# Kernel tuning notes

Measured on AMD Instinct MI355X. Metric: run time of the kernel, lower is better.

## Reference

```python
import jax, jax.numpy as jnp
import numpy as np

NUM_HEADS = 8
NEG_INF = float(-2**32 + 1)  # matches torch padding value -2**32+1


def positional_encoding(B, T, d):
    # matches module: pe[:, :, 0::2] = sin(pos*div), pe[:, :, 1::2] = cos(pos*div)
    pos = jnp.arange(T, dtype=jnp.float32)[:, None]                      # (T, 1)
    div = jnp.exp(jnp.arange(0, d, 2, dtype=jnp.float32) * (-np.log(10000.0) / d))  # (d/2,)
    ang = pos * div                                                       # (T, d/2)
    pe = jnp.zeros((T, d), jnp.float32)
    pe = pe.at[:, 0::2].set(jnp.sin(ang)).at[:, 1::2].set(jnp.cos(ang))
    return jnp.broadcast_to(pe[None], (B, T, d))


def setup_inputs() -> dict:
    key = jax.random.key(0)
    ks = jax.random.split(key, 8)
    B, T, d, dff = 4, 2048, 128, 512
    s = 1.0 / np.sqrt(d)
    return {
        "x": jax.random.normal(ks[0], (B, T, d), jnp.float32),
        "W_Q": jax.random.normal(ks[1], (d, d), jnp.float32) * s,
        "W_K": jax.random.normal(ks[2], (d, d), jnp.float32) * s,
        "W_V": jax.random.normal(ks[3], (d, d), jnp.float32) * s,
        "W1": jax.random.normal(ks[4], (d, dff), jnp.float32) * s,
        "b1": jnp.zeros((dff,), jnp.float32),
        "W2": jax.random.normal(ks[5], (dff, d), jnp.float32) * (1.0 / np.sqrt(dff)),
        "b2": jnp.zeros((d,), jnp.float32),
    }


def reference(x, W_Q, W_K, W_V, W1, b1, W2, b2):
    B, T, d = x.shape
    H = NUM_HEADS
    e = d // H
    x = x + positional_encoding(B, T, d)           # residual later uses post-PE input
    Q = x @ W_Q
    K = x @ W_K
    V = x @ W_V
    # torch split(dim=2)+cat(dim=0) == (b t (h e)) -> (h b) t e; keep head axis separate
    Qh = Q.reshape(B, T, H, e).transpose(2, 0, 1, 3)   # (H, B, T, e)
    Kh = K.reshape(B, T, H, e).transpose(2, 0, 1, 3)
    Vh = V.reshape(B, T, H, e).transpose(2, 0, 1, 3)
    scores = jnp.einsum('hbqe,hbke->hbqk', Qh, Kh) / (T ** 0.5)  # scale by sqrt(time_step)
    mask = jnp.tril(jnp.ones((T, T), jnp.float32))
    scores = jnp.where(mask == 0, jnp.float32(NEG_INF), scores)
    # torch F.softmax(dim=1) on (H*B, T, T) -> softmax over QUERY axis (axis=2 here)
    attn = jax.nn.softmax(scores, axis=2)
    out = jnp.einsum('hbqk,hbke->hbqe', attn, Vh)      # (H, B, T, e)
    out = out.transpose(1, 2, 0, 3).reshape(B, T, d)   # cat heads back on feature dim
    ff = jnp.maximum(out @ W1 + b1, 0.0) @ W2 + b2
    return ff + x
```

## Files before the change

### kernel.cpp

```cpp
#include <hip/hip_runtime.h>
#include <math.h>
#include <stdint.h>

#define T_SEQ 2048
#define BATCH 4
#define DMODEL 128
#define DFF 512
#define NHEAD 8
#define EHEAD 16

#define QSCALE (0.022097086912079608f * 1.4426950408889634f)

typedef __attribute__((ext_vector_type(8))) short bf16x8;
typedef __attribute__((ext_vector_type(4))) short bf16x4;
typedef __attribute__((ext_vector_type(4))) float f32x4;

__device__ __forceinline__ short f2bf(float f) {
    uint32_t u = __float_as_uint(f);
    u = u + 0x7FFF + ((u >> 16) & 1);
    return (short)(u >> 16);
}
__device__ __forceinline__ short bftrunc(float f) {
    return (short)(__float_as_uint(f) >> 16);
}
__device__ __forceinline__ float bf2f(short s) {
    return __uint_as_float(((uint32_t)(unsigned short)s) << 16);
}
__device__ __forceinline__ float exp2_fast(float x) {
#if __has_builtin(__builtin_amdgcn_exp2f)
    return __builtin_amdgcn_exp2f(x);
#else
    float r; asm("v_exp_f32 %0, %1" : "=v"(r) : "v"(x)); return r;
#endif
}

#define MFMA16(A, B, C) __builtin_amdgcn_mfma_f32_16x16x32_bf16(A, B, C, 0, 0, 0)

__device__ __forceinline__ void gload16(const void* g, void* l) {
    __builtin_amdgcn_global_load_lds(
        (const __attribute__((address_space(1))) void*)g,
        (__attribute__((address_space(3))) void*)l, 16, 0, 0);
}

__device__ __forceinline__ int quad_rank(int id) {
    int group = id >> 8, pos = id & 255;
    return (group & 1) ? (((group + 1) << 8) - 1 - pos) : ((group << 8) + pos);
}

#define WP 136
__global__ __launch_bounds__(256) void k_qkv(const float* __restrict__ x,
                                             const float* __restrict__ WQ,
                                             const float* __restrict__ WK,
                                             const float* __restrict__ WV,
                                             const float* __restrict__ W1,
                                             const float* __restrict__ W2,
                                             float* __restrict__ xpe,
                                             short* __restrict__ Qh,
                                             short* __restrict__ Kh,
                                             short* __restrict__ Vs,
                                             short* __restrict__ W1t,
                                             short* __restrict__ W2t) {
    __shared__ __align__(16) short Wlds[128 * WP];
    int z = blockIdx.y;
    int tid = threadIdx.x;

    if (z == 3) {
        int base = (int)blockIdx.x * 256 + tid;
#pragma unroll
        for (int i = 0; i < 2; ++i) {
            int o = base + i * 32768;
            int n = o >> 7, k = o & 127;
            W1t[o] = f2bf(W1[k * 512 + n]);
        }
#pragma unroll
        for (int i = 0; i < 2; ++i) {
            int o = base + i * 32768;
            int n = o >> 9, k = o & 511;
            W2t[o] = f2bf(W2[k * 128 + n]);
        }
        return;
    }

    int wave = tid >> 6, lane = tid & 63;
    int g = lane >> 4, c = lane & 15;
    int row0 = blockIdx.x * 64 + wave * 16;
    int row = row0 + c;
    int tloc = row & (T_SEQ - 1);

    {
        const float* Wsrc = (z == 0) ? WQ : (z == 1) ? WK : WV;
        int k = tid & 127, n0 = (tid >> 7) * 64;
        const float* src = Wsrc + k * 128 + n0;
#pragma unroll
        for (int j = 0; j < 64; j += 4) {
            float4 wv = *(const float4*)(src + j);
            Wlds[(n0 + j + 0) * WP + k] = f2bf(wv.x);
            Wlds[(n0 + j + 1) * WP + k] = f2bf(wv.y);
            Wlds[(n0 + j + 2) * WP + k] = f2bf(wv.z);
            Wlds[(n0 + j + 3) * WP + k] = f2bf(wv.w);
        }
    }

    bf16x8 af[4];
#pragma unroll
    for (int kk = 0; kk < 4; ++kk) {
        int d0 = kk * 32 + 8 * g;
        const float* xb = x + (size_t)row * 128 + d0;
        float4 xa = *(const float4*)(xb);
        float4 xc = *(const float4*)(xb + 4);
        float vv[8] = {xa.x, xa.y, xa.z, xa.w, xc.x, xc.y, xc.z, xc.w};
#pragma unroll
        for (int p = 0; p < 4; ++p) {
            int d = d0 + 2 * p;
            float dv = __expf(-(float)d * (9.210340371976184f / 128.0f));
            float ang = (float)tloc * dv;
            vv[2 * p] += __sinf(ang);
            vv[2 * p + 1] += __cosf(ang);
        }
        if (z == 0) {
            float* xo = xpe + (size_t)row * 128 + d0;
            *(float4*)(xo) = make_float4(vv[0], vv[1], vv[2], vv[3]);
            *(float4*)(xo + 4) = make_float4(vv[4], vv[5], vv[6], vv[7]);
        }
#pragma unroll
        for (int j = 0; j < 8; ++j) af[kk][j] = f2bf(vv[j]);
    }
    __syncthreads();

    bf16x8 wf[8][4];
#pragma unroll
    for (int nt = 0; nt < 8; ++nt)
#pragma unroll
        for (int kk = 0; kk < 4; ++kk)
            wf[nt][kk] = *(const bf16x8*)(&Wlds[(nt * 16 + c) * WP + kk * 32 + 8 * g]);

    f32x4 acc[8];
#pragma unroll
    for (int nt = 0; nt < 8; ++nt) acc[nt] = (f32x4){0.f, 0.f, 0.f, 0.f};
#pragma unroll
    for (int kk = 0; kk < 4; ++kk)
#pragma unroll
        for (int nt = 0; nt < 8; ++nt)
            acc[nt] = MFMA16(af[kk], wf[nt][kk], acc[nt]);

    int b = row0 >> 11;
    int t0 = (row0 & (T_SEQ - 1)) + 4 * g;
    if (z < 2) {
        short* dst = (z == 0) ? Qh : Kh;
        float sc = (z == 0) ? QSCALE : 1.0f;
#pragma unroll
        for (int nt = 0; nt < 8; ++nt) {
            int hb = nt * 4 + b;
#pragma unroll
            for (int r = 0; r < 4; ++r)
                dst[(size_t)(hb * T_SEQ + t0 + r) * 16 + c] = f2bf(acc[nt][r] * sc);
        }
    } else {
#pragma unroll
        for (int nt = 0; nt < 8; ++nt) {
            int hb = nt * 4 + b;
            bf16x4 v;
#pragma unroll
            for (int r = 0; r < 4; ++r) v[r] = f2bf(acc[nt][r]);
            *(bf16x4*)(Vs + (size_t)(hb * 16 + c) * T_SEQ + t0) = v;
        }
    }
}
#undef WP

__global__ __launch_bounds__(256, 4) void k_csum(const short* __restrict__ Qh,
                                                 const short* __restrict__ Kh,
                                                 short* __restrict__ Vs) {
    __shared__ __align__(16) short Qt[2][4096];
    __shared__ float csLds[4][32];
    __shared__ float invl[64];
    const bf16x8 zz = {0, 0, 0, 0, 0, 0, 0, 0};
    const f32x4 z = {0.f, 0.f, 0.f, 0.f};

    int rank = quad_rank((int)blockIdx.x);
    int kc = rank >> 5, hb = rank & 31;
    int tid = threadIdx.x;
    int wave = tid >> 6, lane = tid & 63;
    int g = lane >> 4, c = lane & 15;
    int s = wave & 1, h = wave >> 1;
    int kw = kc * 64 + s * 32;
    const size_t hbT = (size_t)hb * T_SEQ;
    const short* Qg = Qh + hbT * 16;

    bf16x8 kfA = zz, kfB = zz;
    if (g < 2) {
        kfA = *(const bf16x8*)(Kh + (hbT + kw + c) * 16 + 8 * g);
        kfB = *(const bf16x8*)(Kh + (hbT + kw + 16 + c) * 16 + 8 * g);
    }

#define QSTAGE(bf, tq)                                                       \
    do {                                                                     \
        const short* src = Qg + (size_t)(tq) * 4096;                         \
        gload16(src + tid * 8, &Qt[bf][tid * 8]);                            \
        gload16(src + 2048 + tid * 8, &Qt[bf][2048 + tid * 8]);              \
    } while (0)

    int tstart = kc >> 2;
    QSTAGE(0, tstart);
    __syncthreads();

    float csA = 0.f, csB = 0.f;
    for (int t = tstart; t < 8; ++t) {
        int buf = (t - tstart) & 1;
        if (t + 1 < 8) QSTAGE(buf ^ 1, t + 1);
        const short* Qtb = &Qt[buf][0];
#pragma unroll
        for (int sj = 0; sj < 4; ++sj) {
            int ss = 4 * h + sj;
            int q32 = t * 256 + ss * 32;
            if (q32 + 31 < kw) continue;
            bf16x8 qfa = zz, qfb = zz;
            if (g < 2) {
                qfa = *(const bf16x8*)(Qtb + (ss * 32 + c) * 16 + g * 8);
                qfb = *(const bf16x8*)(Qtb + (ss * 32 + 16 + c) * 16 + g * 8);
            }
            f32x4 sA1 = MFMA16(qfa, kfA, z);
            f32x4 sB1 = MFMA16(qfa, kfB, z);
            f32x4 sA2 = MFMA16(qfb, kfA, z);
            f32x4 sB2 = MFMA16(qfb, kfB, z);
            if (q32 >= kw + 32) {
#pragma unroll
                for (int r = 0; r < 4; ++r) {
                    csA += exp2_fast(sA1[r]) + exp2_fast(sA2[r]);
                    csB += exp2_fast(sB1[r]) + exp2_fast(sB2[r]);
                }
            } else {
                int kA = kw + c, kB = kw + 16 + c;
#pragma unroll
                for (int r = 0; r < 4; ++r) {
                    int qa = q32 + 4 * g + r, qb = q32 + 16 + 4 * g + r;
                    csA += (qa >= kA) ? exp2_fast(sA1[r]) : 0.f;
                    csA += (qb >= kA) ? exp2_fast(sA2[r]) : 0.f;
                    csB += (qa >= kB) ? exp2_fast(sB1[r]) : 0.f;
                    csB += (qb >= kB) ? exp2_fast(sB2[r]) : 0.f;
                }
            }
        }
        __syncthreads();
    }
#undef QSTAGE

    csA += __shfl_xor(csA, 16);
    csA += __shfl_xor(csA, 32);
    csB += __shfl_xor(csB, 16);
    csB += __shfl_xor(csB, 32);
    if (lane < 32) csLds[wave][lane] = (lane < 16) ? csA : csB;
    __syncthreads();
    if (tid < 64) {
        int st = tid >> 5, col = tid & 31;
        invl[tid] = 1.0f / (csLds[st][col] + csLds[st + 2][col]);
    }
    __syncthreads();
    if (tid < 128) {
        int e = tid >> 3, kcol = (tid & 7) * 8;
        size_t vo = (size_t)(hb * 16 + e) * T_SEQ + kc * 64 + kcol;
        bf16x8 v = *(bf16x8*)(Vs + vo);
        bf16x8 o;
#pragma unroll
        for (int j = 0; j < 8; ++j) o[j] = f2bf(bf2f(v[j]) * invl[kcol + j]);
        *(bf16x8*)(Vs + vo) = o;
    }
}

__global__ __launch_bounds__(256, 4) void k_attn(const short* __restrict__ Qh,
                                                 const short* __restrict__ Kh,
                                                 const short* __restrict__ Vs,
                                                 short* __restrict__ AObf) {
    __shared__ __align__(16) short Kt[2][4096];
    __shared__ __align__(16) short Vt[2][4096];
    const bf16x8 zz = {0, 0, 0, 0, 0, 0, 0, 0};
    const f32x4 z = {0.f, 0.f, 0.f, 0.f};

    int rank = quad_rank((int)blockIdx.x);
    int qn = 31 - (rank >> 5), hb = rank & 31;
    int h2 = hb >> 2, b = hb & 3;
    int tid = threadIdx.x;
    int wave = tid >> 6, lane = tid & 63;
    int g = lane >> 4, c = lane & 15;
    int s = wave & 1, h = wave >> 1;
    int q0w = qn * 64 + s * 32;
    const size_t hbT = (size_t)hb * T_SEQ;
    const short* Kg = Kh + hbT * 16;
    const short* Vg = Vs + (size_t)hb * 16 * T_SEQ;

    bf16x8 qf0 = zz, qf1 = zz;
    if (g < 2) {
        qf0 = *(const bf16x8*)(Qh + (hbT + q0w + c) * 16 + 8 * g);
        qf1 = *(const bf16x8*)(Qh + (hbT + q0w + 16 + c) * 16 + 8 * g);
    }

    int nT = (qn >> 2) + 1;

#define STAGE(bf, kt)                                                        \
    do {                                                                     \
        int k0s = (kt) * 256;                                                \
        gload16(Kg + (size_t)k0s * 16 + tid * 8, &Kt[bf][tid * 8]);          \
        gload16(Kg + (size_t)k0s * 16 + 2048 + tid * 8,                      \
                &Kt[bf][2048 + tid * 8]);                                    \
        int e0 = tid >> 5, j0 = (tid & 31) ^ (e0 & 7);                       \
        gload16(Vg + (size_t)e0 * T_SEQ + k0s + j0 * 8, &Vt[bf][tid * 8]);   \
        int s1_ = tid + 256;                                                 \
        int e1 = s1_ >> 5, j1 = (s1_ & 31) ^ (e1 & 7);                       \
        gload16(Vg + (size_t)e1 * T_SEQ + k0s + j1 * 8,                      \
                &Vt[bf][2048 + tid * 8]);                                    \
    } while (0)

    STAGE(0, 0);
    __syncthreads();

    f32x4 acc0 = z, acc1 = z;
    for (int t = 0; t < nT; ++t) {
        int buf = t & 1;
        if (t + 1 < nT) STAGE(buf ^ 1, t + 1);
        const short* Ktb = &Kt[buf][0];
        const short* Vtb = &Vt[buf][0];
#pragma unroll
        for (int sj = 0; sj < 4; ++sj) {
            int ss = 4 * h + sj;
            int k32 = t * 256 + ss * 32;
            if (k32 > q0w + 31) continue;
            bf16x8 kf0 = zz, kf1 = zz;
            if (g < 2) {
                kf0 = *(const bf16x8*)(Ktb + (ss * 32 + c) * 16 + g * 8);
                kf1 = *(const bf16x8*)(Ktb + (ss * 32 + 16 + c) * 16 + g * 8);
            }
            int ja = ss * 4 + (g >> 1);
            const short* vrow = Vtb + c * 256 + ((g & 1) << 2);
            bf16x4 v0 = *(const bf16x4*)(vrow + ((ja ^ (c & 7)) << 3));
            bf16x4 v1 = *(const bf16x4*)(vrow + (((ja + 2) ^ (c & 7)) << 3));
            f32x4 s0 = MFMA16(kf0, qf0, z);
            f32x4 s1 = MFMA16(kf1, qf0, z);
            f32x4 s2 = MFMA16(kf0, qf1, z);
            f32x4 s3 = MFMA16(kf1, qf1, z);
            bf16x8 aA, aB, vf;
            if (k32 + 31 <= q0w) {
#pragma unroll
                for (int r = 0; r < 4; ++r) {
                    aA[r] = bftrunc(exp2_fast(s0[r]));
                    aA[4 + r] = bftrunc(exp2_fast(s1[r]));
                    aB[r] = bftrunc(exp2_fast(s2[r]));
                    aB[4 + r] = bftrunc(exp2_fast(s3[r]));
                    vf[r] = v0[r];
                    vf[4 + r] = v1[r];
                }
            } else {
                int qa = q0w + c, qb = q0w + 16 + c;
                int ka = k32 + 4 * g, kb = k32 + 16 + 4 * g;
#pragma unroll
                for (int r = 0; r < 4; ++r) {
                    aA[r] = (ka + r <= qa) ? bftrunc(exp2_fast(s0[r])) : (short)0;
                    aA[4 + r] = (kb + r <= qa) ? bftrunc(exp2_fast(s1[r])) : (short)0;
                    aB[r] = (ka + r <= qb) ? bftrunc(exp2_fast(s2[r])) : (short)0;
                    aB[4 + r] = (kb + r <= qb) ? bftrunc(exp2_fast(s3[r])) : (short)0;
                    vf[r] = v0[r];
                    vf[4 + r] = v1[r];
                }
            }
            acc0 = MFMA16(aA, vf, acc0);
            acc1 = MFMA16(aB, vf, acc1);
        }
        __syncthreads();
    }
#undef STAGE

    float* Of = (float*)&Kt[0][0];
    if (h == 1) {
#pragma unroll
        for (int r = 0; r < 4; ++r) {
            Of[r * 128 + s * 64 + lane] = acc0[r];
            Of[(4 + r) * 128 + s * 64 + lane] = acc1[r];
        }
    }
    __syncthreads();
    if (h == 0) {
#pragma unroll
        for (int r = 0; r < 4; ++r) {
            acc0[r] += Of[r * 128 + s * 64 + lane];
            acc1[r] += Of[(4 + r) * 128 + s * 64 + lane];
        }
#pragma unroll
        for (int r = 0; r < 4; ++r) {
            AObf[(size_t)(b * T_SEQ + q0w + 4 * g + r) * DMODEL + h2 * EHEAD + c] = f2bf(acc0[r]);
            AObf[(size_t)(b * T_SEQ + q0w + 16 + 4 * g + r) * DMODEL + h2 * EHEAD + c] = f2bf(acc1[r]);
        }
    }
}

__global__ __launch_bounds__(256) void k_ff(const short* __restrict__ AObf,
                                            const short* __restrict__ W1t,
                                            const float* __restrict__ b1,
                                            const short* __restrict__ W2t,
                                            const float* __restrict__ b2,
                                            const float* __restrict__ xpe,
                                            float* __restrict__ out) {
    __shared__ __align__(16) short Fl[32][516];
    int w = threadIdx.x >> 6, lane = threadIdx.x & 63;
    int g = lane >> 4, c = lane & 15;
    int row0 = blockIdx.x * 32;

    {
        bf16x8 wf[8][4];
#pragma unroll
        for (int nt = 0; nt < 8; ++nt)
#pragma unroll
            for (int kk = 0; kk < 4; ++kk)
                wf[nt][kk] = *(const bf16x8*)(W1t + (w * 128 + nt * 16 + c) * 128 + kk * 32 + 8 * g);

#pragma unroll
        for (int ch = 0; ch < 2; ++ch) {
            int rbase = row0 + ch * 16;
            bf16x8 af[4];
#pragma unroll
            for (int kk = 0; kk < 4; ++kk)
                af[kk] = *(const bf16x8*)(AObf + (size_t)(rbase + c) * 128 + kk * 32 + 8 * g);

            f32x4 acc[8];
#pragma unroll
            for (int nt = 0; nt < 8; ++nt) acc[nt] = (f32x4){0.f, 0.f, 0.f, 0.f};
#pragma unroll
            for (int kk = 0; kk < 4; ++kk)
#pragma unroll
                for (int nt = 0; nt < 8; ++nt)
                    acc[nt] = MFMA16(af[kk], wf[nt][kk], acc[nt]);

#pragma unroll
            for (int nt = 0; nt < 8; ++nt) {
                int col = w * 128 + nt * 16 + c;
                float bb = b1[col];
#pragma unroll
                for (int r = 0; r < 4; ++r)
                    Fl[ch * 16 + 4 * g + r][col] = f2bf(fmaxf(acc[nt][r] + bb, 0.f));
            }
        }
    }
    __syncthreads();

    bf16x8 wf2[2][16];
#pragma unroll
    for (int nt = 0; nt < 2; ++nt)
#pragma unroll
        for (int kk = 0; kk < 16; ++kk)
            wf2[nt][kk] = *(const bf16x8*)(W2t + (w * 32 + nt * 16 + c) * 512 + kk * 32 + 8 * g);

#pragma unroll
    for (int ch = 0; ch < 2; ++ch) {
        int rbase = row0 + ch * 16;
        f32x4 acc2[2];
        acc2[0] = (f32x4){0.f, 0.f, 0.f, 0.f};
        acc2[1] = (f32x4){0.f, 0.f, 0.f, 0.f};
#pragma unroll
        for (int kk = 0; kk < 16; ++kk) {
            bf16x8 a = *(const bf16x8*)(&Fl[ch * 16 + c][kk * 32 + 8 * g]);
            acc2[0] = MFMA16(a, wf2[0][kk], acc2[0]);
            acc2[1] = MFMA16(a, wf2[1][kk], acc2[1]);
        }
#pragma unroll
        for (int nt = 0; nt < 2; ++nt) {
            int col = w * 32 + nt * 16 + c;
            float bb = b2[col];
#pragma unroll
            for (int r = 0; r < 4; ++r) {
                size_t o = (size_t)(rbase + 4 * g + r) * DMODEL + col;
                out[o] = acc2[nt][r] + bb + xpe[o];
            }
        }
    }
}

extern "C" void kernel_launch(void* const* d_in, const int* in_sizes, int n_in,
                              void* d_out, int out_size, void* d_ws, size_t ws_size,
                              hipStream_t stream) {
    const float* x  = (const float*)d_in[0];
    const float* WQ = (const float*)d_in[1];
    const float* WK = (const float*)d_in[2];
    const float* WV = (const float*)d_in[3];
    const float* W1 = (const float*)d_in[4];
    const float* b1 = (const float*)d_in[5];
    const float* W2 = (const float*)d_in[6];
    const float* b2 = (const float*)d_in[7];
    float* out = (float*)d_out;

    const size_t NTD = (size_t)BATCH * T_SEQ * DMODEL;
    float* xpe   = (float*)d_ws;
    short* Qh    = (short*)(xpe + NTD);
    short* Kh    = Qh + NTD;
    short* Vs    = Kh + NTD;
    short* AObf  = Vs + NTD;
    short* W1t   = AObf + NTD;
    short* W2t   = W1t + 65536;

    k_qkv<<<dim3(128, 4), dim3(256), 0, stream>>>(x, WQ, WK, WV, W1, W2,
                                                  xpe, Qh, Kh, Vs, W1t, W2t);

    k_csum<<<dim3(1024), dim3(256), 0, stream>>>(Qh, Kh, Vs);

    k_attn<<<dim3(1024), dim3(256), 0, stream>>>(Qh, Kh, Vs, AObf);

    k_ff<<<dim3(256), dim3(256), 0, stream>>>(AObf, W1t, b1, W2t, b2, xpe, out);
}
```

Before: 55.08 us.

## Halve per-block work in csum and attention kernels, doubling grid to 2048 blocks

```diff
diff --git a/kernel.cpp b/kernel.cpp
--- a/kernel.cpp
+++ b/kernel.cpp
@@ -42,7 +42,7 @@
         (__attribute__((address_space(3))) void*)l, 16, 0, 0);
 }
 
-__device__ __forceinline__ int quad_rank(int id) {
+__device__ __forceinline__ int oct_rank(int id) {
     int group = id >> 8, pos = id & 255;
     return (group & 1) ? (((group + 1) << 8) - 1 - pos) : ((group << 8) + pos);
 }
@@ -173,17 +173,16 @@
                                                  short* __restrict__ Vs) {
     __shared__ __align__(16) short Qt[2][4096];
     __shared__ float csLds[4][32];
-    __shared__ float invl[64];
+    __shared__ float invl[32];
     const bf16x8 zz = {0, 0, 0, 0, 0, 0, 0, 0};
     const f32x4 z = {0.f, 0.f, 0.f, 0.f};
 
-    int rank = quad_rank((int)blockIdx.x);
+    int rank = oct_rank((int)blockIdx.x);
     int kc = rank >> 5, hb = rank & 31;
     int tid = threadIdx.x;
     int wave = tid >> 6, lane = tid & 63;
     int g = lane >> 4, c = lane & 15;
-    int s = wave & 1, h = wave >> 1;
-    int kw = kc * 64 + s * 32;
+    int kw = kc * 32;
     const size_t hbT = (size_t)hb * T_SEQ;
     const short* Qg = Qh + hbT * 16;
 
@@ -200,7 +199,7 @@
         gload16(src + 2048 + tid * 8, &Qt[bf][2048 + tid * 8]);              \
     } while (0)
 
-    int tstart = kc >> 2;
+    int tstart = kc >> 3;
     QSTAGE(0, tstart);
     __syncthreads();
 
@@ -210,8 +209,8 @@
         if (t + 1 < 8) QSTAGE(buf ^ 1, t + 1);
         const short* Qtb = &Qt[buf][0];
 #pragma unroll
-        for (int sj = 0; sj < 4; ++sj) {
-            int ss = 4 * h + sj;
+        for (int sj = 0; sj < 2; ++sj) {
+            int ss = 2 * wave + sj;
             int q32 = t * 256 + ss * 32;
             if (q32 + 31 < kw) continue;
             bf16x8 qfa = zz, qfb = zz;
@@ -251,18 +250,17 @@
     csB += __shfl_xor(csB, 32);
     if (lane < 32) csLds[wave][lane] = (lane < 16) ? csA : csB;
     __syncthreads();
+    if (tid < 32)
+        invl[tid] = 1.0f / (csLds[0][tid] + csLds[1][tid] +
+                            csLds[2][tid] + csLds[3][tid]);
+    __syncthreads();
     if (tid < 64) {
-        int st = tid >> 5, col = tid & 31;
-        invl[tid] = 1.0f / (csLds[st][col] + csLds[st + 2][col]);
-    }
-    __syncthreads();
-    if (tid < 128) {
-        int e = tid >> 3, kcol = (tid & 7) * 8;
-        size_t vo = (size_t)(hb * 16 + e) * T_SEQ + kc * 64 + kcol;
+        int e = tid >> 2, kg = tid & 3;
+        size_t vo = (size_t)(hb * 16 + e) * T_SEQ + kw + kg * 8;
         bf16x8 v = *(bf16x8*)(Vs + vo);
         bf16x8 o;
 #pragma unroll
-        for (int j = 0; j < 8; ++j) o[j] = f2bf(bf2f(v[j]) * invl[kcol + j]);
+        for (int j = 0; j < 8; ++j) o[j] = f2bf(bf2f(v[j]) * invl[kg * 8 + j]);
         *(bf16x8*)(Vs + vo) = o;
     }
 }
@@ -271,19 +269,19 @@
                                                  const short* __restrict__ Kh,
                                                  const short* __restrict__ Vs,
                                                  short* __restrict__ AObf) {
-    __shared__ __align__(16) short Kt[2][4096];
-    __shared__ __align__(16) short Vt[2][4096];
+    __shared__ __align__(16) short Kt[2][2048];
+    __shared__ __align__(16) short Vt[2][2048];
     const bf16x8 zz = {0, 0, 0, 0, 0, 0, 0, 0};
     const f32x4 z = {0.f, 0.f, 0.f, 0.f};
 
-    int rank = quad_rank((int)blockIdx.x);
-    int qn = 31 - (rank >> 5), hb = rank & 31;
+    int rank = oct_rank((int)blockIdx.x);
+    int strip = rank >> 5;
+    int q0w = (63 - strip) * 32;
+    int hb = rank & 31;
     int h2 = hb >> 2, b = hb & 3;
     int tid = threadIdx.x;
     int wave = tid >> 6, lane = tid & 63;
     int g = lane >> 4, c = lane & 15;
-    int s = wave & 1, h = wave >> 1;
-    int q0w = qn * 64 + s * 32;
     const size_t hbT = (size_t)hb * T_SEQ;
     const short* Kg = Kh + hbT * 16;
     const short* Vg = Vs + (size_t)hb * 16 * T_SEQ;
@@ -294,20 +292,14 @@
         qf1 = *(const bf16x8*)(Qh + (hbT + q0w + 16 + c) * 16 + 8 * g);
     }
 
-    int nT = (qn >> 2) + 1;
+    int nT = (q0w >> 7) + 1;
 
 #define STAGE(bf, kt)                                                        \
     do {                                                                     \
-        int k0s = (kt) * 256;                                                \
+        int k0s = (kt) * 128;                                                \
         gload16(Kg + (size_t)k0s * 16 + tid * 8, &Kt[bf][tid * 8]);          \
-        gload16(Kg + (size_t)k0s * 16 + 2048 + tid * 8,                      \
-                &Kt[bf][2048 + tid * 8]);                                    \
-        int e0 = tid >> 5, j0 = (tid & 31) ^ (e0 & 7);                       \
+        int e0 = tid >> 4, jp = tid & 15, j0 = jp ^ (e0 & 7);                \
         gload16(Vg + (size_t)e0 * T_SEQ + k0s + j0 * 8, &Vt[bf][tid * 8]);   \
-        int s1_ = tid + 256;                                                 \
-        int e1 = s1_ >> 5, j1 = (s1_ & 31) ^ (e1 & 7);                       \
-        gload16(Vg + (size_t)e1 * T_SEQ + k0s + j1 * 8,                      \
-                &Vt[bf][2048 + tid * 8]);                                    \
     } while (0)
 
     STAGE(0, 0);
@@ -319,18 +311,16 @@
         if (t + 1 < nT) STAGE(buf ^ 1, t + 1);
         const short* Ktb = &Kt[buf][0];
         const short* Vtb = &Vt[buf][0];
-#pragma unroll
-        for (int sj = 0; sj < 4; ++sj) {
-            int ss = 4 * h + sj;
-            int k32 = t * 256 + ss * 32;
-            if (k32 > q0w + 31) continue;
+        int ss = wave;
+        int k32 = t * 128 + ss * 32;
+        if (k32 <= q0w + 31) {
             bf16x8 kf0 = zz, kf1 = zz;
             if (g < 2) {
                 kf0 = *(const bf16x8*)(Ktb + (ss * 32 + c) * 16 + g * 8);
                 kf1 = *(const bf16x8*)(Ktb + (ss * 32 + 16 + c) * 16 + g * 8);
             }
             int ja = ss * 4 + (g >> 1);
-            const short* vrow = Vtb + c * 256 + ((g & 1) << 2);
+            const short* vrow = Vtb + c * 128 + ((g & 1) << 2);
             bf16x4 v0 = *(const bf16x4*)(vrow + ((ja ^ (c & 7)) << 3));
             bf16x4 v1 = *(const bf16x4*)(vrow + (((ja + 2) ^ (c & 7)) << 3));
             f32x4 s0 = MFMA16(kf0, qf0, z);
@@ -369,19 +359,22 @@
 #undef STAGE
 
     float* Of = (float*)&Kt[0][0];
-    if (h == 1) {
+    if (wave > 0) {
 #pragma unroll
         for (int r = 0; r < 4; ++r) {
-            Of[r * 128 + s * 64 + lane] = acc0[r];
-            Of[(4 + r) * 128 + s * 64 + lane] = acc1[r];
-        }
-    }
-    __syncthreads();
-    if (h == 0) {
+            Of[((wave - 1) * 8 + r) * 64 + lane] = acc0[r];
+            Of[((wave - 1) * 8 + 4 + r) * 64 + lane] = acc1[r];
+        }
+    }
+    __syncthreads();
+    if (wave == 0) {
 #pragma unroll
         for (int r = 0; r < 4; ++r) {
-            acc0[r] += Of[r * 128 + s * 64 + lane];
-            acc1[r] += Of[(4 + r) * 128 + s * 64 + lane];
+#pragma unroll
+            for (int w = 1; w < 4; ++w) {
+                acc0[r] += Of[((w - 1) * 8 + r) * 64 + lane];
+                acc1[r] += Of[((w - 1) * 8 + 4 + r) * 64 + lane];
+            }
         }
 #pragma unroll
         for (int r = 0; r < 4; ++r) {
@@ -497,9 +490,9 @@
     k_qkv<<<dim3(128, 4), dim3(256), 0, stream>>>(x, WQ, WK, WV, W1, W2,
                                                   xpe, Qh, Kh, Vs, W1t, W2t);
 
-    k_csum<<<dim3(1024), dim3(256), 0, stream>>>(Qh, Kh, Vs);
-
-    k_attn<<<dim3(1024), dim3(256), 0, stream>>>(Qh, Kh, Vs, AObf);
+    k_csum<<<dim3(2048), dim3(256), 0, stream>>>(Qh, Kh, Vs);
+
+    k_attn<<<dim3(2048), dim3(256), 0, stream>>>(Qh, Kh, Vs, AObf);
 
     k_ff<<<dim3(256), dim3(256), 0, stream>>>(AObf, W1t, b1, W2t, b2, xpe, out);
 }
```

New measurement: 55.00 us (median of 2 runs). Within noise of the previous version (-0.2%).
